# Optimization experiments

Hardware: AMD Instinct MI355X
Metric: run time of the kernel (lower is better)

Reference implementation:

```python
import jax, jax.numpy as jnp
import numpy as np

EPS = 1e-5

def conv2d(x, w, b=None, pad=1):
    # x: [B,C,H,W], w: [O,I,kh,kw]
    y = jax.lax.conv_general_dilated(x, w, (1, 1), [(pad, pad), (pad, pad)],
                                     dimension_numbers=('NCHW', 'OIHW', 'NCHW'))
    if b is not None:
        y = y + b[None, :, None, None]
    return y

def bn(x, g, b, m, v):
    # inference-mode batchnorm
    inv = g / jnp.sqrt(v + EPS)
    return x * inv[None, :, None, None] + (b - m * inv)[None, :, None, None]

def coord_conv(x, w, b):
    B, C, H, W = x.shape
    yy = jnp.broadcast_to(jnp.linspace(-1.0, 1.0, H)[:, None], (H, W))
    xx = jnp.broadcast_to(jnp.linspace(-1.0, 1.0, W)[None, :], (H, W))
    coords = jnp.broadcast_to(jnp.stack([xx, yy])[None], (B, 2, H, W)).astype(x.dtype)
    return conv2d(jnp.concatenate([x, coords], axis=1), w, b, pad=1)

def deform_conv(x, offset, w):
    # deformable conv v1, 3x3, pad=1, stride=1, no bias
    B, C, H, W = x.shape
    K = 9
    # offset channels interleaved (y, x) per kernel tap
    off = offset.reshape(B, K, 2, H, W)
    off_y, off_x = off[:, :, 0], off[:, :, 1]          # [B,9,H,W]
    k = jnp.arange(K)
    ko_y = (k // 3 - 1).astype(x.dtype)[None, :, None, None]
    ko_x = (k % 3 - 1).astype(x.dtype)[None, :, None, None]
    base_y = jnp.arange(H, dtype=x.dtype)[None, None, :, None]
    base_x = jnp.arange(W, dtype=x.dtype)[None, None, None, :]
    py = base_y + ko_y + off_y                          # [B,9,H,W]
    px = base_x + ko_x + off_x
    xf = x.reshape(B, C, H * W)
    y0 = jnp.floor(py)
    x0 = jnp.floor(px)
    acc = jnp.zeros((B, C, K, H, W), x.dtype)
    for dy in (0.0, 1.0):
        for dx in (0.0, 1.0):
            yy = y0 + dy
            xx = x0 + dx
            wgt = (1.0 - jnp.abs(py - yy)) * (1.0 - jnp.abs(px - xx))
            valid = (yy >= 0) & (yy < H) & (xx >= 0) & (xx < W)
            wgt = jnp.where(valid, wgt, 0.0)            # zero padding OOB
            yi = jnp.clip(yy, 0, H - 1).astype(jnp.int32)
            xi = jnp.clip(xx, 0, W - 1).astype(jnp.int32)
            idx = (yi * W + xi).reshape(B, K * H * W)
            v = jnp.take_along_axis(xf, idx[:, None, :], axis=2).reshape(B, C, K, H, W)
            acc = acc + v * wgt[:, None]
    wk = w.reshape(w.shape[0], w.shape[1], K)           # [O,I,9]
    return jnp.einsum('bckhw,ock->bohw', acc, wk)

def setup_inputs() -> dict:
    key = jax.random.key(0)
    ks = jax.random.split(key, 16)
    d_model, hd = 256, 64
    B, H, W = 8, 96, 96
    f32 = jnp.float32
    def bn_params(k):
        k1, k2, k3 = jax.random.split(k, 3)
        return (1.0 + 0.1 * jax.random.normal(k1, (hd,), f32),
                0.1 * jax.random.normal(k2, (hd,), f32),
                0.1 * jax.random.normal(k3, (hd,), f32),
                0.5 + jax.random.uniform(jax.random.fold_in(k, 7), (hd,), f32))
    bn1 = bn_params(ks[1]); bn2 = bn_params(ks[2]); bn3 = bn_params(ks[3]); bn4 = bn_params(ks[4])
    inp = {
        'features': jax.random.normal(ks[0], (B, H, W, d_model), f32),
        'coord_w': 0.05 * jax.random.normal(ks[5], (hd, d_model + 2, 3, 3), f32),
        'coord_b': jnp.zeros((hd,), f32),
        'bn1_g': bn1[0], 'bn1_b': bn1[1], 'bn1_m': bn1[2], 'bn1_v': bn1[3],
        'off_w': 0.01 * jax.random.normal(ks[6], (18, hd, 3, 3), f32),
        'off_b': 0.01 * jax.random.normal(ks[7], (18,), f32),
        'dc_w': 0.05 * jax.random.normal(ks[8], (hd, hd, 3, 3), f32),
        'bn2_g': bn2[0], 'bn2_b': bn2[1], 'bn2_m': bn2[2], 'bn2_v': bn2[3],
        'r1_w': 0.05 * jax.random.normal(ks[9], (hd, hd, 3, 3), f32),
        'bn3_g': bn3[0], 'bn3_b': bn3[1], 'bn3_m': bn3[2], 'bn3_v': bn3[3],
        'r2_w': 0.05 * jax.random.normal(ks[10], (hd, hd, 3, 3), f32),
        'bn4_g': bn4[0], 'bn4_b': bn4[1], 'bn4_m': bn4[2], 'bn4_v': bn4[3],
        'out_w': 0.1 * jax.random.normal(ks[11], (1, hd, 1, 1), f32),
        'out_b': jnp.zeros((1,), f32),
    }
    return inp

def reference(features, coord_w, coord_b, bn1_g, bn1_b, bn1_m, bn1_v,
              off_w, off_b, dc_w, bn2_g, bn2_b, bn2_m, bn2_v,
              r1_w, bn3_g, bn3_b, bn3_m, bn3_v,
              r2_w, bn4_g, bn4_b, bn4_m, bn4_v, out_w, out_b):
    x = jnp.transpose(features, (0, 3, 1, 2))           # NHWC -> NCHW
    x = jax.nn.relu(bn(coord_conv(x, coord_w, coord_b), bn1_g, bn1_b, bn1_m, bn1_v))
    offset = conv2d(x, off_w, off_b, pad=1)
    x = deform_conv(x, offset, dc_w)
    x = jax.nn.relu(bn(x, bn2_g, bn2_b, bn2_m, bn2_v))
    x = jax.nn.relu(bn(conv2d(x, r1_w, None, pad=1), bn3_g, bn3_b, bn3_m, bn3_v))
    x = jax.nn.relu(bn(conv2d(x, r2_w, None, pad=1), bn4_g, bn4_b, bn4_m, bn4_v))
    return jax.nn.sigmoid(conv2d(x, out_w, out_b, pad=0))
```

## Files before the change

kernel.cpp:

```cpp
#include <hip/hip_runtime.h>


typedef unsigned short u16;
typedef unsigned int u32;
typedef __attribute__((ext_vector_type(8)))  short bf16x8;
typedef __attribute__((ext_vector_type(16))) float f32x16;

#define EPSBN 1e-5f

__device__ __forceinline__ u16 f2bf(float f) {
  u32 u = __builtin_bit_cast(u32, f);
  u32 r = u + 0x7FFFu + ((u >> 16) & 1u);
  return (u16)(r >> 16);
}
__device__ __forceinline__ u32 pk2(float a, float b) {
  return (u32)f2bf(a) | ((u32)f2bf(b) << 16);
}
__device__ __forceinline__ float lo2f(u32 w) { return __builtin_bit_cast(float, w << 16); }
__device__ __forceinline__ float hi2f(u32 w) { return __builtin_bit_cast(float, w & 0xFFFF0000u); }

#define N_WCF 147456
#define N_WCC 9216
#define N_WOF 18432
#define N_W64 36864
#define N_ALLW (N_WCF + N_WCC + N_WOF + 3*N_W64)

__global__ __launch_bounds__(256) void prep_kernel(
    const float* __restrict__ coord_w, const float* __restrict__ off_w,
    const float* __restrict__ dc_w, const float* __restrict__ r1_w,
    const float* __restrict__ r2_w,
    u16* __restrict__ wcf, u16* __restrict__ wcc, u16* __restrict__ wof,
    u16* __restrict__ wdf, u16* __restrict__ wr1, u16* __restrict__ wr2)
{
  int i = blockIdx.x * 256 + threadIdx.x;
  if (i >= N_ALLW) return;
  int d = i;
  if (d < N_WCF) {
    int j = d & 7, lane = (d >> 3) & 63, frag = d >> 9;
    int nt = frag & 1, h = (frag >> 1) & 3, tap = (frag >> 3) % 9, cc = (frag >> 3) / 9;
    int ic = cc * 64 + h * 16 + ((lane >> 5) << 3) + j;
    int oc = nt * 32 + (lane & 31);
    wcf[d] = f2bf(coord_w[((size_t)oc * 258 + ic) * 9 + tap]);
    return;
  }
  d -= N_WCF;
  if (d < N_WCC) {
    int j = d & 7, lane = (d >> 3) & 63, frag = d >> 9;
    int nt = frag & 1, tap = frag >> 1;
    int ic = 256 + ((lane >> 5) << 3) + j;
    int oc = nt * 32 + (lane & 31);
    wcc[d] = (ic < 258) ? f2bf(coord_w[((size_t)oc * 258 + ic) * 9 + tap]) : (u16)0;
    return;
  }
  d -= N_WCC;
  if (d < N_WOF) {
    int j = d & 7, lane = (d >> 3) & 63, frag = d >> 9;
    int h = frag & 3, tap = frag >> 2;
    int ic = h * 16 + ((lane >> 5) << 3) + j;
    int oc = lane & 31;
    wof[d] = (oc < 18) ? f2bf(off_w[((size_t)oc * 64 + ic) * 9 + tap]) : (u16)0;
    return;
  }
  d -= N_WOF;
  int seg = d / N_W64;
  int e = d - seg * N_W64;
  int j = e & 7, lane = (e >> 3) & 63, frag = e >> 9;
  int nt = frag & 1, h = (frag >> 1) & 3, tap = frag >> 3;
  int ic = h * 16 + ((lane >> 5) << 3) + j;
  int oc = nt * 32 + (lane & 31);
  const float* src = (seg == 0) ? dc_w : (seg == 1) ? r1_w : r2_w;
  u16* dst = (seg == 0) ? wdf : (seg == 1) ? wr1 : wr2;
  dst[e] = f2bf(src[((size_t)oc * 64 + ic) * 9 + tap]);
}

__global__ __launch_bounds__(256, 4) void coord_conv_kernel(
    const float* __restrict__ feat, const u16* __restrict__ wcf,
    const u16* __restrict__ wcc, const float* __restrict__ cb,
    const float* __restrict__ g, const float* __restrict__ bb,
    const float* __restrict__ m, const float* __restrict__ v,
    u16* __restrict__ x1b)
{
  __shared__ __align__(16) u16 tile[6 * 34 * 72];
  const int t = threadIdx.x;
  const int wv = t >> 6, lane = t & 63;
  const int l31 = lane & 31, l5 = lane >> 5;
  const int x0 = blockIdx.x * 32, y0 = blockIdx.y * 4, b = blockIdx.z;

  f32x16 acc[2] = {};

  for (int cc = 0; cc < 4; ++cc) {
    __syncthreads();
    for (int i = t; i < 1632; i += 256) {
      const int px = i >> 3, gg = i & 7;
      const int ly = px / 34, lx = px - ly * 34;
      const int gy = y0 + ly - 1, gx = x0 + lx - 1;
      uint4 o = {0u, 0u, 0u, 0u};
      if ((unsigned)gy < 96u && (unsigned)gx < 96u) {
        const float* p = feat + ((size_t)((b * 96 + gy) * 96 + gx)) * 256
                         + cc * 64 + gg * 8;
        const float4 f0 = *(const float4*)p;
        const float4 f1 = *(const float4*)(p + 4);
        o.x = pk2(f0.x, f0.y); o.y = pk2(f0.z, f0.w);
        o.z = pk2(f1.x, f1.y); o.w = pk2(f1.z, f1.w);
      }
      *(uint4*)(tile + (ly * 34 + lx) * 72 + gg * 8) = o;
    }
    __syncthreads();
    #pragma unroll
    for (int tap = 0; tap < 9; ++tap) {
      const int dy = tap / 3, dx = tap - dy * 3;
      #pragma unroll
      for (int h = 0; h < 4; ++h) {
        const bf16x8 afr = *(const bf16x8*)(tile +
            ((wv + dy) * 34 + l31 + dx) * 72 + h * 16 + l5 * 8);
        #pragma unroll
        for (int nt = 0; nt < 2; ++nt) {
          const bf16x8 bfr = *(const bf16x8*)(wcf +
              ((size_t)((((cc * 9 + tap) * 4 + h) * 2) + nt)) * 512 + lane * 8);
          acc[nt] = __builtin_amdgcn_mfma_f32_32x32x16_bf16(afr, bfr, acc[nt],
                                                            0, 0, 0);
        }
      }
    }
  }

  __syncthreads();
  for (int i = t; i < 408; i += 256) {
    const int px = i >> 1, gg = i & 1;
    const int ly = px / 34, lx = px - ly * 34;
    const int gy = y0 + ly - 1, gx = x0 + lx - 1;
    uint4 o = {0u, 0u, 0u, 0u};
    if (gg == 0 && (unsigned)gy < 96u && (unsigned)gx < 96u) {
      const float xx = -1.f + (2.f / 95.f) * (float)gx;
      const float yy = -1.f + (2.f / 95.f) * (float)gy;
      o.x = pk2(xx, yy);
    }
    *(uint4*)(tile + (ly * 34 + lx) * 72 + gg * 8) = o;
  }
  __syncthreads();
  #pragma unroll
  for (int tap = 0; tap < 9; ++tap) {
    const int dy = tap / 3, dx = tap - dy * 3;
    const bf16x8 afr = *(const bf16x8*)(tile +
        ((wv + dy) * 34 + l31 + dx) * 72 + l5 * 8);
    #pragma unroll
    for (int nt = 0; nt < 2; ++nt) {
      const bf16x8 bfr = *(const bf16x8*)(wcc +
          ((size_t)(tap * 2 + nt)) * 512 + lane * 8);
      acc[nt] = __builtin_amdgcn_mfma_f32_32x32x16_bf16(afr, bfr, acc[nt],
                                                        0, 0, 0);
    }
  }

  const int y = y0 + wv;
  #pragma unroll
  for (int nt = 0; nt < 2; ++nt) {
    const int oc = nt * 32 + l31;
    const float inv = g[oc] * rsqrtf(v[oc] + EPSBN);
    const float sh = bb[oc] - m[oc] * inv + cb[oc] * inv;
    #pragma unroll
    for (int r = 0; r < 16; ++r) {
      const int xr = (r & 3) + 8 * (r >> 2) + 4 * l5;
      const float val = fmaxf(fmaf(acc[nt][r], inv, sh), 0.f);
      x1b[((size_t)((b * 96 + y) * 96 + x0 + xr)) * 64 + oc] = f2bf(val);
    }
  }
}

template<int NN, int EPI>
__global__ __launch_bounds__(256, 4) void conv64_kernel(
    const u16* __restrict__ xin, const u16* __restrict__ wf,
    const float* __restrict__ bias,
    const float* __restrict__ g, const float* __restrict__ bb,
    const float* __restrict__ m, const float* __restrict__ v,
    const float* __restrict__ ow, const float* __restrict__ ob,
    void* __restrict__ outp)
{
  __shared__ __align__(16) u16 tile[6 * 34 * 72];
  __shared__ float red[128];
  const int t = threadIdx.x;
  const int wv = t >> 6, lane = t & 63;
  const int l31 = lane & 31, l5 = lane >> 5;
  const int x0 = blockIdx.x * 32, y0 = blockIdx.y * 4, b = blockIdx.z;

  for (int i = t; i < 1632; i += 256) {
    const int px = i >> 3, gg = i & 7;
    const int ly = px / 34, lx = px - ly * 34;
    const int gy = y0 + ly - 1, gx = x0 + lx - 1;
    uint4 o = {0u, 0u, 0u, 0u};
    if ((unsigned)gy < 96u && (unsigned)gx < 96u)
      o = *(const uint4*)(xin + (((size_t)((b * 96 + gy) * 96 + gx)) << 6)
                          + gg * 8);
    *(uint4*)(tile + (ly * 34 + lx) * 72 + gg * 8) = o;
  }
  __syncthreads();

  f32x16 acc[NN] = {};
  #pragma unroll
  for (int tap = 0; tap < 9; ++tap) {
    const int dy = tap / 3, dx = tap - dy * 3;
    #pragma unroll
    for (int h = 0; h < 4; ++h) {
      const bf16x8 afr = *(const bf16x8*)(tile +
          ((wv + dy) * 34 + l31 + dx) * 72 + h * 16 + l5 * 8);
      #pragma unroll
      for (int nt = 0; nt < NN; ++nt) {
        const bf16x8 bfr = *(const bf16x8*)(wf +
            ((size_t)((tap * 4 + h) * NN + nt)) * 512 + lane * 8);
        acc[nt] = __builtin_amdgcn_mfma_f32_32x32x16_bf16(afr, bfr, acc[nt],
                                                          0, 0, 0);
      }
    }
  }

  const int y = y0 + wv;
  if constexpr (EPI == 0) {
    u16* xo = (u16*)outp;
    #pragma unroll
    for (int nt = 0; nt < NN; ++nt) {
      const int oc = nt * 32 + l31;
      const float inv = g[oc] * rsqrtf(v[oc] + EPSBN);
      const float sh = bb[oc] - m[oc] * inv;
      #pragma unroll
      for (int r = 0; r < 16; ++r) {
        const int xr = (r & 3) + 8 * (r >> 2) + 4 * l5;
        const float val = fmaxf(fmaf(acc[nt][r], inv, sh), 0.f);
        xo[((size_t)((b * 96 + y) * 96 + x0 + xr)) * 64 + oc] = f2bf(val);
      }
    }
  } else if constexpr (EPI == 1) {
    float* fo = (float*)outp;
    const int oc = l31;
    if (oc < 18) {
      const float bs = bias[oc];
      #pragma unroll
      for (int r = 0; r < 16; ++r) {
        const int xr = (r & 3) + 8 * (r >> 2) + 4 * l5;
        fo[((size_t)((b * 96 + y) * 96 + x0 + xr)) * 18 + oc] = acc[0][r] + bs;
      }
    }
  } else {
    float pr[16];
    #pragma unroll
    for (int r = 0; r < 16; ++r) pr[r] = 0.f;
    #pragma unroll
    for (int nt = 0; nt < NN; ++nt) {
      const int oc = nt * 32 + l31;
      const float inv = g[oc] * rsqrtf(v[oc] + EPSBN);
      const float sh = bb[oc] - m[oc] * inv;
      const float wo = ow[oc];
      #pragma unroll
      for (int r = 0; r < 16; ++r) {
        const float val = fmaxf(fmaf(acc[nt][r], inv, sh), 0.f);
        pr[r] = fmaf(val, wo, pr[r]);
      }
    }
    #pragma unroll
    for (int mask = 1; mask <= 16; mask <<= 1)
      #pragma unroll
      for (int r = 0; r < 16; ++r)
        pr[r] += __shfl_xor(pr[r], mask);
    if (l31 == 0) {
      #pragma unroll
      for (int r = 0; r < 16; ++r) {
        const int xr = (r & 3) + 8 * (r >> 2) + 4 * l5;
        red[wv * 32 + xr] = pr[r];
      }
    }
    __syncthreads();
    if (t < 128) {
      float* fo = (float*)outp;
      const int yy = y0 + (t >> 5), xx = x0 + (t & 31);
      const float val = red[t] + ob[0];
      fo[(size_t)(b * 96 + yy) * 96 + xx] = 1.f / (1.f + expf(-val));
    }
  }
}

__global__ __launch_bounds__(256, 4) void deform_kernel(
    const u16* __restrict__ x1b, const float* __restrict__ off,
    const u16* __restrict__ wdf,
    const float* __restrict__ g, const float* __restrict__ bb,
    const float* __restrict__ m, const float* __restrict__ v,
    u16* __restrict__ x2b)
{
  __shared__ __align__(16) u16 s[128 * 72];
  __shared__ float offs[128 * 18];
  const int t = threadIdx.x;
  const int wv = t >> 6, lane = t & 63;
  const int l31 = lane & 31, l5 = lane >> 5;
  const int x0 = blockIdx.x * 16, y0 = blockIdx.y * 8, b = blockIdx.z;

  for (int i = t; i < 2304; i += 256) {
    const int p = i / 18, c = i - p * 18;
    const int gy = y0 + (p >> 4), gx = x0 + (p & 15);
    offs[i] = off[((size_t)((b * 96 + gy) * 96 + gx)) * 18 + c];
  }

  f32x16 acc[2] = {};

  for (int k = 0; k < 9; ++k) {
    __syncthreads();
    #pragma unroll
    for (int rr = 0; rr < 2; ++rr) {
      const int role = t + rr * 256;
      const int sp = role >> 2, part = role & 3;
      const int sy = y0 + (sp >> 4), sx = x0 + (sp & 15);
      const float oy = offs[sp * 18 + 2 * k];
      const float ox = offs[sp * 18 + 2 * k + 1];
      const float py = (float)(sy + k / 3 - 1) + oy;
      const float px = (float)(sx + k % 3 - 1) + ox;
      const float yf = floorf(py), xf = floorf(px);
      const float fy = py - yf, fx = px - xf;
      const int yi = (int)yf, xi = (int)xf;
      float val[16];
      #pragma unroll
      for (int j = 0; j < 16; ++j) val[j] = 0.f;
      #pragma unroll
      for (int cor = 0; cor < 4; ++cor) {
        const int cy = yi + (cor >> 1), cx = xi + (cor & 1);
        if ((unsigned)cy < 96u && (unsigned)cx < 96u) {
          const float wy = (cor & 2) ? fy : 1.f - fy;
          const float wx = (cor & 1) ? fx : 1.f - fx;
          const float wgt = wy * wx;
          const u16* sp2 = x1b + ((size_t)((b * 96 + cy) * 96 + cx)) * 64
                           + part * 16;
          const uint4 ua = *(const uint4*)sp2;
          const uint4 ub = *(const uint4*)(sp2 + 8);
          const u32 uu[8] = {ua.x, ua.y, ua.z, ua.w, ub.x, ub.y, ub.z, ub.w};
          #pragma unroll
          for (int u = 0; u < 8; ++u) {
            val[2 * u]     = fmaf(wgt, lo2f(uu[u]), val[2 * u]);
            val[2 * u + 1] = fmaf(wgt, hi2f(uu[u]), val[2 * u + 1]);
          }
        }
      }
      u32 pk[8];
      #pragma unroll
      for (int u = 0; u < 8; ++u) pk[u] = pk2(val[2 * u], val[2 * u + 1]);
      uint4 w0 = {pk[0], pk[1], pk[2], pk[3]};
      uint4 w1 = {pk[4], pk[5], pk[6], pk[7]};
      *(uint4*)(s + sp * 72 + part * 16) = w0;
      *(uint4*)(s + sp * 72 + part * 16 + 8) = w1;
    }
    __syncthreads();
    #pragma unroll
    for (int h = 0; h < 4; ++h) {
      const bf16x8 afr = *(const bf16x8*)(s + (wv * 32 + l31) * 72
                                          + h * 16 + l5 * 8);
      #pragma unroll
      for (int nt = 0; nt < 2; ++nt) {
        const bf16x8 bfr = *(const bf16x8*)(wdf +
            ((size_t)((k * 4 + h) * 2 + nt)) * 512 + lane * 8);
        acc[nt] = __builtin_amdgcn_mfma_f32_32x32x16_bf16(afr, bfr, acc[nt],
                                                          0, 0, 0);
      }
    }
  }

  #pragma unroll
  for (int nt = 0; nt < 2; ++nt) {
    const int oc = nt * 32 + l31;
    const float inv = g[oc] * rsqrtf(v[oc] + EPSBN);
    const float sh = bb[oc] - m[oc] * inv;
    #pragma unroll
    for (int r = 0; r < 16; ++r) {
      const int pxi = wv * 32 + (r & 3) + 8 * (r >> 2) + 4 * l5;
      const int y = y0 + (pxi >> 4), x = x0 + (pxi & 15);
      const float val = fmaxf(fmaf(acc[nt][r], inv, sh), 0.f);
      x2b[((size_t)((b * 96 + y) * 96 + x)) * 64 + oc] = f2bf(val);
    }
  }
}

extern "C" void kernel_launch(void* const* d_in, const int* in_sizes, int n_in,
                              void* d_out, int out_size, void* d_ws,
                              size_t ws_size, hipStream_t stream)
{
  (void)in_sizes; (void)n_in; (void)out_size; (void)ws_size;
  const float* features = (const float*)d_in[0];
  const float* coord_w  = (const float*)d_in[1];
  const float* coord_b  = (const float*)d_in[2];
  const float* bn1g = (const float*)d_in[3];
  const float* bn1b = (const float*)d_in[4];
  const float* bn1m = (const float*)d_in[5];
  const float* bn1v = (const float*)d_in[6];
  const float* off_w = (const float*)d_in[7];
  const float* off_b = (const float*)d_in[8];
  const float* dc_w  = (const float*)d_in[9];
  const float* bn2g = (const float*)d_in[10];
  const float* bn2b = (const float*)d_in[11];
  const float* bn2m = (const float*)d_in[12];
  const float* bn2v = (const float*)d_in[13];
  const float* r1_w = (const float*)d_in[14];
  const float* bn3g = (const float*)d_in[15];
  const float* bn3b = (const float*)d_in[16];
  const float* bn3m = (const float*)d_in[17];
  const float* bn3v = (const float*)d_in[18];
  const float* r2_w = (const float*)d_in[19];
  const float* bn4g = (const float*)d_in[20];
  const float* bn4b = (const float*)d_in[21];
  const float* bn4m = (const float*)d_in[22];
  const float* bn4v = (const float*)d_in[23];
  const float* out_w = (const float*)d_in[24];
  const float* out_b = (const float*)d_in[25];

  char* W = (char*)d_ws;
  float* offb = (float*)W;
  u16*   x1b  = (u16*)(W + 5308416);
  u16*   x2b  = (u16*)(W + 14745600);
  u16*   x3b  = (u16*)(W + 24182784);
  u16*   wcf  = (u16*)(W + 33619968);
  u16*   wcc  = wcf + N_WCF;
  u16*   wof  = wcc + N_WCC;
  u16*   wdf  = wof + N_WOF;
  u16*   wr1  = wdf + N_W64;
  u16*   wr2  = wr1 + N_W64;

  prep_kernel<<<(N_ALLW + 255) / 256, 256, 0, stream>>>(
      coord_w, off_w, dc_w, r1_w, r2_w, wcf, wcc, wof, wdf, wr1, wr2);

  dim3 grid(3, 24, 8);
  dim3 gridD(6, 12, 8);

  coord_conv_kernel<<<grid, 256, 0, stream>>>(
      features, wcf, wcc, coord_b, bn1g, bn1b, bn1m, bn1v, x1b);
  conv64_kernel<1, 1><<<grid, 256, 0, stream>>>(
      x1b, wof, off_b, nullptr, nullptr, nullptr, nullptr, nullptr, nullptr,
      (void*)offb);
  deform_kernel<<<gridD, 256, 0, stream>>>(
      x1b, offb, wdf, bn2g, bn2b, bn2m, bn2v, x2b);
  conv64_kernel<2, 0><<<grid, 256, 0, stream>>>(
      x2b, wr1, nullptr, bn3g, bn3b, bn3m, bn3v, nullptr, nullptr, (void*)x3b);
  conv64_kernel<2, 2><<<grid, 256, 0, stream>>>(
      x3b, wr2, nullptr, bn4g, bn4b, bn4m, bn4v, out_w, out_b, d_out);
}
```

Measured before the change: 270.8 us.

## Fuse offset conv into deform kernel, precompute coord channels, double-buffer loads

Several changes land together. The coordinate-channel part of the coord conv is precomputed once into a per-pixel table in the prep kernel rather than run as extra MFMA work. The offset conv is fused into the deform kernel through a shared-memory halo, which removes one launch and the global offset buffer. All conv kernels move to 512 threads, with each wave owning one output-channel tile. The coord conv and the deform gather gain register-staged double buffering so loads overlap the MFMA work. The trade-offs are more register pressure, shared-memory atomics in the final reduction, and a larger prep kernel.

```diff
diff --git a/kernel.cpp b/kernel.cpp
--- a/kernel.cpp
+++ b/kernel.cpp
@@ -19,21 +19,31 @@
 __device__ __forceinline__ float lo2f(u32 w) { return __builtin_bit_cast(float, w << 16); }
 __device__ __forceinline__ float hi2f(u32 w) { return __builtin_bit_cast(float, w & 0xFFFF0000u); }
 
+#define O_X1   0u
+#define O_X2   9437184u
+#define O_X3   18874368u
+#define O_PRE  28311552u
+#define O_WCF  30670848u
+#define O_WOF  30965760u
+#define O_WDF  31002624u
+#define O_WR1  31076352u
+#define O_WR2  31150080u
+
 #define N_WCF 147456
-#define N_WCC 9216
 #define N_WOF 18432
 #define N_W64 36864
-#define N_ALLW (N_WCF + N_WCC + N_WOF + 3*N_W64)
+#define N_PRE 589824
+#define N_TOT (N_WCF + N_WOF + 3*N_W64 + N_PRE)
 
 __global__ __launch_bounds__(256) void prep_kernel(
-    const float* __restrict__ coord_w, const float* __restrict__ off_w,
-    const float* __restrict__ dc_w, const float* __restrict__ r1_w,
-    const float* __restrict__ r2_w,
-    u16* __restrict__ wcf, u16* __restrict__ wcc, u16* __restrict__ wof,
-    u16* __restrict__ wdf, u16* __restrict__ wr1, u16* __restrict__ wr2)
+    const float* __restrict__ coord_w, const float* __restrict__ coord_b,
+    const float* __restrict__ off_w, const float* __restrict__ dc_w,
+    const float* __restrict__ r1_w, const float* __restrict__ r2_w,
+    u16* __restrict__ wcf, u16* __restrict__ wof, u16* __restrict__ wdf,
+    u16* __restrict__ wr1, u16* __restrict__ wr2, float* __restrict__ pre)
 {
   int i = blockIdx.x * 256 + threadIdx.x;
-  if (i >= N_ALLW) return;
+  if (i >= N_TOT) return;
   int d = i;
   if (d < N_WCF) {
     int j = d & 7, lane = (d >> 3) & 63, frag = d >> 9;
@@ -44,15 +54,6 @@
     return;
   }
   d -= N_WCF;
-  if (d < N_WCC) {
-    int j = d & 7, lane = (d >> 3) & 63, frag = d >> 9;
-    int nt = frag & 1, tap = frag >> 1;
-    int ic = 256 + ((lane >> 5) << 3) + j;
-    int oc = nt * 32 + (lane & 31);
-    wcc[d] = (ic < 258) ? f2bf(coord_w[((size_t)oc * 258 + ic) * 9 + tap]) : (u16)0;
-    return;
-  }
-  d -= N_WCC;
   if (d < N_WOF) {
     int j = d & 7, lane = (d >> 3) & 63, frag = d >> 9;
     int h = frag & 3, tap = frag >> 2;
@@ -62,199 +63,203 @@
     return;
   }
   d -= N_WOF;
-  int seg = d / N_W64;
-  int e = d - seg * N_W64;
-  int j = e & 7, lane = (e >> 3) & 63, frag = e >> 9;
-  int nt = frag & 1, h = (frag >> 1) & 3, tap = frag >> 3;
-  int ic = h * 16 + ((lane >> 5) << 3) + j;
-  int oc = nt * 32 + (lane & 31);
-  const float* src = (seg == 0) ? dc_w : (seg == 1) ? r1_w : r2_w;
-  u16* dst = (seg == 0) ? wdf : (seg == 1) ? wr1 : wr2;
-  dst[e] = f2bf(src[((size_t)oc * 64 + ic) * 9 + tap]);
-}
-
-__global__ __launch_bounds__(256, 4) void coord_conv_kernel(
+  if (d < 3 * N_W64) {
+    int seg = d / N_W64;
+    int e = d - seg * N_W64;
+    int j = e & 7, lane = (e >> 3) & 63, frag = e >> 9;
+    int nt = frag & 1, h = (frag >> 1) & 3, tap = frag >> 3;
+    int ic = h * 16 + ((lane >> 5) << 3) + j;
+    int oc = nt * 32 + (lane & 31);
+    const float* src = (seg == 0) ? dc_w : (seg == 1) ? r1_w : r2_w;
+    u16* dst = (seg == 0) ? wdf : (seg == 1) ? wr1 : wr2;
+    dst[e] = f2bf(src[((size_t)oc * 64 + ic) * 9 + tap]);
+    return;
+  }
+  d -= 3 * N_W64;
+  int oc = d & 63;
+  int r = d >> 6;
+  int x = r % 96, y = r / 96;
+  float s = coord_b[oc];
+  #pragma unroll
+  for (int tap = 0; tap < 9; ++tap) {
+    const int dy = tap / 3, dx = tap - dy * 3;
+    const int sy = y + dy - 1, sx = x + dx - 1;
+    if ((unsigned)sy < 96u && (unsigned)sx < 96u) {
+      const float xx = -1.f + (2.f / 95.f) * (float)sx;
+      const float yy = -1.f + (2.f / 95.f) * (float)sy;
+      s += coord_w[((size_t)oc * 258 + 256) * 9 + tap] * xx
+         + coord_w[((size_t)oc * 258 + 257) * 9 + tap] * yy;
+    }
+  }
+  pre[((size_t)(y * 96 + x) << 6) + oc] = s;
+}
+
+__global__ __launch_bounds__(512, 4) void coord_conv_kernel(
     const float* __restrict__ feat, const u16* __restrict__ wcf,
-    const u16* __restrict__ wcc, const float* __restrict__ cb,
+    const float* __restrict__ pre,
     const float* __restrict__ g, const float* __restrict__ bb,
     const float* __restrict__ m, const float* __restrict__ v,
     u16* __restrict__ x1b)
 {
-  __shared__ __align__(16) u16 tile[6 * 34 * 72];
+  __shared__ __align__(16) u16 buf[2][204 * 72];
   const int t = threadIdx.x;
   const int wv = t >> 6, lane = t & 63;
   const int l31 = lane & 31, l5 = lane >> 5;
+  const int row = wv >> 1, nt = wv & 1;
   const int x0 = blockIdx.x * 32, y0 = blockIdx.y * 4, b = blockIdx.z;
 
-  f32x16 acc[2] = {};
-
+  int rpx[4], rgg[4]; size_t rgo[4]; bool rok[4], ract[4];
+  #pragma unroll
+  for (int it = 0; it < 4; ++it) {
+    int r = t + it * 512;
+    ract[it] = (r < 1632);
+    int px = r >> 3; if (px > 203) px = 203;
+    rgg[it] = r & 7;
+    rpx[it] = px;
+    int ly = px / 34, lx = px - ly * 34;
+    int gy = y0 + ly - 1, gx = x0 + lx - 1;
+    rok[it] = ract[it] && ((unsigned)gy < 96u) && ((unsigned)gx < 96u);
+    rgo[it] = ((size_t)((b * 96 + gy) * 96 + gx)) * 256 + rgg[it] * 8;
+  }
+
+  float4 ra[4][2];
+  #pragma unroll
+  for (int it = 0; it < 4; ++it) {
+    ra[it][0] = make_float4(0.f, 0.f, 0.f, 0.f);
+    ra[it][1] = make_float4(0.f, 0.f, 0.f, 0.f);
+    if (rok[it]) {
+      const float* p = feat + rgo[it];
+      ra[it][0] = *(const float4*)p;
+      ra[it][1] = *(const float4*)(p + 4);
+    }
+  }
+  #pragma unroll
+  for (int it = 0; it < 4; ++it) if (ract[it]) {
+    uint4 o = {pk2(ra[it][0].x, ra[it][0].y), pk2(ra[it][0].z, ra[it][0].w),
+               pk2(ra[it][1].x, ra[it][1].y), pk2(ra[it][1].z, ra[it][1].w)};
+    *(uint4*)(&buf[0][rpx[it] * 72 + rgg[it] * 8]) = o;
+  }
+  __syncthreads();
+
+  f32x16 acc = {};
   for (int cc = 0; cc < 4; ++cc) {
-    __syncthreads();
-    for (int i = t; i < 1632; i += 256) {
-      const int px = i >> 3, gg = i & 7;
-      const int ly = px / 34, lx = px - ly * 34;
-      const int gy = y0 + ly - 1, gx = x0 + lx - 1;
-      uint4 o = {0u, 0u, 0u, 0u};
-      if ((unsigned)gy < 96u && (unsigned)gx < 96u) {
-        const float* p = feat + ((size_t)((b * 96 + gy) * 96 + gx)) * 256
-                         + cc * 64 + gg * 8;
-        const float4 f0 = *(const float4*)p;
-        const float4 f1 = *(const float4*)(p + 4);
-        o.x = pk2(f0.x, f0.y); o.y = pk2(f0.z, f0.w);
-        o.z = pk2(f1.x, f1.y); o.w = pk2(f1.z, f1.w);
-      }
-      *(uint4*)(tile + (ly * 34 + lx) * 72 + gg * 8) = o;
-    }
-    __syncthreads();
+    const int cur = cc & 1;
+    if (cc < 3) {
+      #pragma unroll
+      for (int it = 0; it < 4; ++it) {
+        ra[it][0] = make_float4(0.f, 0.f, 0.f, 0.f);
+        ra[it][1] = make_float4(0.f, 0.f, 0.f, 0.f);
+        if (rok[it]) {
+          const float* p = feat + rgo[it] + (size_t)(cc + 1) * 64;
+          ra[it][0] = *(const float4*)p;
+          ra[it][1] = *(const float4*)(p + 4);
+        }
+      }
+    }
     #pragma unroll
     for (int tap = 0; tap < 9; ++tap) {
       const int dy = tap / 3, dx = tap - dy * 3;
       #pragma unroll
       for (int h = 0; h < 4; ++h) {
-        const bf16x8 afr = *(const bf16x8*)(tile +
-            ((wv + dy) * 34 + l31 + dx) * 72 + h * 16 + l5 * 8);
-        #pragma unroll
-        for (int nt = 0; nt < 2; ++nt) {
-          const bf16x8 bfr = *(const bf16x8*)(wcf +
-              ((size_t)((((cc * 9 + tap) * 4 + h) * 2) + nt)) * 512 + lane * 8);
-          acc[nt] = __builtin_amdgcn_mfma_f32_32x32x16_bf16(afr, bfr, acc[nt],
-                                                            0, 0, 0);
-        }
-      }
-    }
-  }
-
-  __syncthreads();
-  for (int i = t; i < 408; i += 256) {
-    const int px = i >> 1, gg = i & 1;
-    const int ly = px / 34, lx = px - ly * 34;
-    const int gy = y0 + ly - 1, gx = x0 + lx - 1;
-    uint4 o = {0u, 0u, 0u, 0u};
-    if (gg == 0 && (unsigned)gy < 96u && (unsigned)gx < 96u) {
-      const float xx = -1.f + (2.f / 95.f) * (float)gx;
-      const float yy = -1.f + (2.f / 95.f) * (float)gy;
-      o.x = pk2(xx, yy);
-    }
-    *(uint4*)(tile + (ly * 34 + lx) * 72 + gg * 8) = o;
-  }
-  __syncthreads();
-  #pragma unroll
-  for (int tap = 0; tap < 9; ++tap) {
-    const int dy = tap / 3, dx = tap - dy * 3;
-    const bf16x8 afr = *(const bf16x8*)(tile +
-        ((wv + dy) * 34 + l31 + dx) * 72 + l5 * 8);
-    #pragma unroll
-    for (int nt = 0; nt < 2; ++nt) {
-      const bf16x8 bfr = *(const bf16x8*)(wcc +
-          ((size_t)(tap * 2 + nt)) * 512 + lane * 8);
-      acc[nt] = __builtin_amdgcn_mfma_f32_32x32x16_bf16(afr, bfr, acc[nt],
-                                                        0, 0, 0);
-    }
-  }
-
-  const int y = y0 + wv;
-  #pragma unroll
-  for (int nt = 0; nt < 2; ++nt) {
-    const int oc = nt * 32 + l31;
-    const float inv = g[oc] * rsqrtf(v[oc] + EPSBN);
-    const float sh = bb[oc] - m[oc] * inv + cb[oc] * inv;
-    #pragma unroll
-    for (int r = 0; r < 16; ++r) {
-      const int xr = (r & 3) + 8 * (r >> 2) + 4 * l5;
-      const float val = fmaxf(fmaf(acc[nt][r], inv, sh), 0.f);
-      x1b[((size_t)((b * 96 + y) * 96 + x0 + xr)) * 64 + oc] = f2bf(val);
-    }
-  }
-}
-
-template<int NN, int EPI>
-__global__ __launch_bounds__(256, 4) void conv64_kernel(
+        const bf16x8 afr = *(const bf16x8*)(
+            &buf[cur][((row + dy) * 34 + l31 + dx) * 72 + h * 16 + l5 * 8]);
+        const bf16x8 bfr = *(const bf16x8*)(
+            wcf + ((size_t)(((cc * 9 + tap) * 4 + h) * 2 + nt)) * 512 + lane * 8);
+        acc = __builtin_amdgcn_mfma_f32_32x32x16_bf16(afr, bfr, acc, 0, 0, 0);
+      }
+    }
+    if (cc < 3) {
+      #pragma unroll
+      for (int it = 0; it < 4; ++it) if (ract[it]) {
+        uint4 o = {pk2(ra[it][0].x, ra[it][0].y), pk2(ra[it][0].z, ra[it][0].w),
+                   pk2(ra[it][1].x, ra[it][1].y), pk2(ra[it][1].z, ra[it][1].w)};
+        *(uint4*)(&buf[1 - cur][rpx[it] * 72 + rgg[it] * 8]) = o;
+      }
+    }
+    __syncthreads();
+  }
+
+  const int oc = nt * 32 + l31;
+  const float inv = g[oc] * rsqrtf(v[oc] + EPSBN);
+  const float sh = bb[oc] - m[oc] * inv;
+  const int y = y0 + row;
+  #pragma unroll
+  for (int r = 0; r < 16; ++r) {
+    const int xr = (r & 3) + 8 * (r >> 2) + 4 * l5;
+    const int x = x0 + xr;
+    const float pv = pre[((size_t)(y * 96 + x) << 6) + oc];
+    const float val = fmaxf(fmaf(acc[r] + pv, inv, sh), 0.f);
+    x1b[(((size_t)((b * 96 + y) * 96 + x)) << 6) + oc] = f2bf(val);
+  }
+}
+
+template<int EPI>
+__global__ __launch_bounds__(512, 4) void conv64_kernel(
     const u16* __restrict__ xin, const u16* __restrict__ wf,
-    const float* __restrict__ bias,
     const float* __restrict__ g, const float* __restrict__ bb,
     const float* __restrict__ m, const float* __restrict__ v,
     const float* __restrict__ ow, const float* __restrict__ ob,
     void* __restrict__ outp)
 {
-  __shared__ __align__(16) u16 tile[6 * 34 * 72];
+  __shared__ __align__(16) u16 tile[204 * 72];
   __shared__ float red[128];
   const int t = threadIdx.x;
   const int wv = t >> 6, lane = t & 63;
   const int l31 = lane & 31, l5 = lane >> 5;
+  const int row = wv >> 1, nt = wv & 1;
   const int x0 = blockIdx.x * 32, y0 = blockIdx.y * 4, b = blockIdx.z;
 
-  for (int i = t; i < 1632; i += 256) {
-    const int px = i >> 3, gg = i & 7;
-    const int ly = px / 34, lx = px - ly * 34;
-    const int gy = y0 + ly - 1, gx = x0 + lx - 1;
-    uint4 o = {0u, 0u, 0u, 0u};
-    if ((unsigned)gy < 96u && (unsigned)gx < 96u)
-      o = *(const uint4*)(xin + (((size_t)((b * 96 + gy) * 96 + gx)) << 6)
-                          + gg * 8);
-    *(uint4*)(tile + (ly * 34 + lx) * 72 + gg * 8) = o;
+  if constexpr (EPI == 2) { if (t < 128) red[t] = 0.f; }
+
+  #pragma unroll
+  for (int it = 0; it < 4; ++it) {
+    int r = t + it * 512;
+    if (r < 1632) {
+      int px = r >> 3, gg = r & 7;
+      int ly = px / 34, lx = px - ly * 34;
+      int gy = y0 + ly - 1, gx = x0 + lx - 1;
+      uint4 o = {0u, 0u, 0u, 0u};
+      if ((unsigned)gy < 96u && (unsigned)gx < 96u)
+        o = *(const uint4*)(xin + (((size_t)((b * 96 + gy) * 96 + gx)) << 6)
+                            + gg * 8);
+      *(uint4*)(&tile[px * 72 + gg * 8]) = o;
+    }
   }
   __syncthreads();
 
-  f32x16 acc[NN] = {};
+  f32x16 acc = {};
   #pragma unroll
   for (int tap = 0; tap < 9; ++tap) {
     const int dy = tap / 3, dx = tap - dy * 3;
     #pragma unroll
     for (int h = 0; h < 4; ++h) {
-      const bf16x8 afr = *(const bf16x8*)(tile +
-          ((wv + dy) * 34 + l31 + dx) * 72 + h * 16 + l5 * 8);
-      #pragma unroll
-      for (int nt = 0; nt < NN; ++nt) {
-        const bf16x8 bfr = *(const bf16x8*)(wf +
-            ((size_t)((tap * 4 + h) * NN + nt)) * 512 + lane * 8);
-        acc[nt] = __builtin_amdgcn_mfma_f32_32x32x16_bf16(afr, bfr, acc[nt],
-                                                          0, 0, 0);
-      }
-    }
-  }
-
-  const int y = y0 + wv;
+      const bf16x8 afr = *(const bf16x8*)(
+          &tile[((row + dy) * 34 + l31 + dx) * 72 + h * 16 + l5 * 8]);
+      const bf16x8 bfr = *(const bf16x8*)(
+          wf + ((size_t)((tap * 4 + h) * 2 + nt)) * 512 + lane * 8);
+      acc = __builtin_amdgcn_mfma_f32_32x32x16_bf16(afr, bfr, acc, 0, 0, 0);
+    }
+  }
+
+  const int oc = nt * 32 + l31;
+  const float inv = g[oc] * rsqrtf(v[oc] + EPSBN);
+  const float sh = bb[oc] - m[oc] * inv;
+  const int y = y0 + row;
+
   if constexpr (EPI == 0) {
     u16* xo = (u16*)outp;
     #pragma unroll
-    for (int nt = 0; nt < NN; ++nt) {
-      const int oc = nt * 32 + l31;
-      const float inv = g[oc] * rsqrtf(v[oc] + EPSBN);
-      const float sh = bb[oc] - m[oc] * inv;
-      #pragma unroll
-      for (int r = 0; r < 16; ++r) {
-        const int xr = (r & 3) + 8 * (r >> 2) + 4 * l5;
-        const float val = fmaxf(fmaf(acc[nt][r], inv, sh), 0.f);
-        xo[((size_t)((b * 96 + y) * 96 + x0 + xr)) * 64 + oc] = f2bf(val);
-      }
-    }
-  } else if constexpr (EPI == 1) {
-    float* fo = (float*)outp;
-    const int oc = l31;
-    if (oc < 18) {
-      const float bs = bias[oc];
-      #pragma unroll
-      for (int r = 0; r < 16; ++r) {
-        const int xr = (r & 3) + 8 * (r >> 2) + 4 * l5;
-        fo[((size_t)((b * 96 + y) * 96 + x0 + xr)) * 18 + oc] = acc[0][r] + bs;
-      }
+    for (int r = 0; r < 16; ++r) {
+      const int xr = (r & 3) + 8 * (r >> 2) + 4 * l5;
+      const float val = fmaxf(fmaf(acc[r], inv, sh), 0.f);
+      xo[(((size_t)((b * 96 + y) * 96 + x0 + xr)) << 6) + oc] = f2bf(val);
     }
   } else {
+    const float wo = ow[oc];
     float pr[16];
     #pragma unroll
-    for (int r = 0; r < 16; ++r) pr[r] = 0.f;
-    #pragma unroll
-    for (int nt = 0; nt < NN; ++nt) {
-      const int oc = nt * 32 + l31;
-      const float inv = g[oc] * rsqrtf(v[oc] + EPSBN);
-      const float sh = bb[oc] - m[oc] * inv;
-      const float wo = ow[oc];
-      #pragma unroll
-      for (int r = 0; r < 16; ++r) {
-        const float val = fmaxf(fmaf(acc[nt][r], inv, sh), 0.f);
-        pr[r] = fmaf(val, wo, pr[r]);
-      }
-    }
+    for (int r = 0; r < 16; ++r)
+      pr[r] = fmaxf(fmaf(acc[r], inv, sh), 0.f) * wo;
     #pragma unroll
     for (int mask = 1; mask <= 16; mask <<= 1)
       #pragma unroll
@@ -264,7 +269,7 @@
       #pragma unroll
       for (int r = 0; r < 16; ++r) {
         const int xr = (r & 3) + 8 * (r >> 2) + 4 * l5;
-        red[wv * 32 + xr] = pr[r];
+        atomicAdd(&red[row * 32 + xr], pr[r]);
       }
     }
     __syncthreads();
@@ -277,99 +282,151 @@
   }
 }
 
-__global__ __launch_bounds__(256, 4) void deform_kernel(
-    const u16* __restrict__ x1b, const float* __restrict__ off,
-    const u16* __restrict__ wdf,
+__global__ __launch_bounds__(512, 4) void offdeform_kernel(
+    const u16* __restrict__ x1b, const u16* __restrict__ wof,
+    const u16* __restrict__ wdf, const float* __restrict__ off_b,
     const float* __restrict__ g, const float* __restrict__ bb,
     const float* __restrict__ m, const float* __restrict__ v,
     u16* __restrict__ x2b)
 {
-  __shared__ __align__(16) u16 s[128 * 72];
-  __shared__ float offs[128 * 18];
+  __shared__ __align__(16) char arena[9216 + 36864];
+  float* offs = (float*)arena;
+  u16* halo = (u16*)(arena + 9216);
+  u16* sb0 = (u16*)(arena + 9216);
+  u16* sb1 = (u16*)(arena + 9216 + 18432);
   const int t = threadIdx.x;
   const int wv = t >> 6, lane = t & 63;
   const int l31 = lane & 31, l5 = lane >> 5;
+  const int mtile = wv >> 1, nt = wv & 1;
   const int x0 = blockIdx.x * 16, y0 = blockIdx.y * 8, b = blockIdx.z;
 
-  for (int i = t; i < 2304; i += 256) {
-    const int p = i / 18, c = i - p * 18;
-    const int gy = y0 + (p >> 4), gx = x0 + (p & 15);
-    offs[i] = off[((size_t)((b * 96 + gy) * 96 + gx)) * 18 + c];
-  }
-
-  f32x16 acc[2] = {};
-
-  for (int k = 0; k < 9; ++k) {
-    __syncthreads();
+  #pragma unroll
+  for (int it = 0; it < 3; ++it) {
+    int r = t + it * 512;
+    if (r < 1440) {
+      int px = r >> 3, gg = r & 7;
+      int hy = px / 18, hx = px - hy * 18;
+      int gy = y0 + hy - 1, gx = x0 + hx - 1;
+      uint4 o = {0u, 0u, 0u, 0u};
+      if ((unsigned)gy < 96u && (unsigned)gx < 96u)
+        o = *(const uint4*)(x1b + (((size_t)((b * 96 + gy) * 96 + gx)) << 6)
+                            + gg * 8);
+      *(uint4*)(&halo[px * 72 + gg * 8]) = o;
+    }
+  }
+  __syncthreads();
+
+  if (wv < 4) {
+    const int om = wv * 32 + l31;
+    const int oy_ = om >> 4, ox_ = om & 15;
+    f32x16 oacc = {};
+    #pragma unroll
+    for (int tap = 0; tap < 9; ++tap) {
+      const int dy = tap / 3, dx = tap - dy * 3;
+      #pragma unroll
+      for (int h = 0; h < 4; ++h) {
+        const bf16x8 afr = *(const bf16x8*)(
+            &halo[((oy_ + dy) * 18 + ox_ + dx) * 72 + h * 16 + l5 * 8]);
+        const bf16x8 bfr = *(const bf16x8*)(
+            wof + ((size_t)(tap * 4 + h)) * 512 + lane * 8);
+        oacc = __builtin_amdgcn_mfma_f32_32x32x16_bf16(afr, bfr, oacc, 0, 0, 0);
+      }
+    }
+    if (l31 < 18) {
+      const float bs = off_b[l31];
+      #pragma unroll
+      for (int r = 0; r < 16; ++r) {
+        const int p = wv * 32 + (r & 3) + 8 * (r >> 2) + 4 * l5;
+        offs[p * 18 + l31] = oacc[r] + bs;
+      }
+    }
+  }
+  __syncthreads();
+
+  const int gg = t & 7, p0 = t >> 3;
+  f32x16 acc = {};
+  uint4 cv[2][4];
+  float cw[2][4];
+
+  auto gather = [&](int k) {
+    const int kdy = k / 3, kdx = k - kdy * 3;
     #pragma unroll
     for (int rr = 0; rr < 2; ++rr) {
-      const int role = t + rr * 256;
-      const int sp = role >> 2, part = role & 3;
-      const int sy = y0 + (sp >> 4), sx = x0 + (sp & 15);
-      const float oy = offs[sp * 18 + 2 * k];
-      const float ox = offs[sp * 18 + 2 * k + 1];
-      const float py = (float)(sy + k / 3 - 1) + oy;
-      const float px = (float)(sx + k % 3 - 1) + ox;
-      const float yf = floorf(py), xf = floorf(px);
-      const float fy = py - yf, fx = px - xf;
+      const int p = p0 + rr * 64;
+      const float oy = offs[p * 18 + 2 * k];
+      const float ox = offs[p * 18 + 2 * k + 1];
+      const float py = (float)(y0 + (p >> 4) + kdy - 1) + oy;
+      const float pxf = (float)(x0 + (p & 15) + kdx - 1) + ox;
+      const float yf = floorf(py), xf = floorf(pxf);
+      const float fy = py - yf, fx = pxf - xf;
       const int yi = (int)yf, xi = (int)xf;
-      float val[16];
-      #pragma unroll
-      for (int j = 0; j < 16; ++j) val[j] = 0.f;
       #pragma unroll
       for (int cor = 0; cor < 4; ++cor) {
         const int cy = yi + (cor >> 1), cx = xi + (cor & 1);
-        if ((unsigned)cy < 96u && (unsigned)cx < 96u) {
-          const float wy = (cor & 2) ? fy : 1.f - fy;
-          const float wx = (cor & 1) ? fx : 1.f - fx;
-          const float wgt = wy * wx;
-          const u16* sp2 = x1b + ((size_t)((b * 96 + cy) * 96 + cx)) * 64
-                           + part * 16;
-          const uint4 ua = *(const uint4*)sp2;
-          const uint4 ub = *(const uint4*)(sp2 + 8);
-          const u32 uu[8] = {ua.x, ua.y, ua.z, ua.w, ub.x, ub.y, ub.z, ub.w};
-          #pragma unroll
-          for (int u = 0; u < 8; ++u) {
-            val[2 * u]     = fmaf(wgt, lo2f(uu[u]), val[2 * u]);
-            val[2 * u + 1] = fmaf(wgt, hi2f(uu[u]), val[2 * u + 1]);
-          }
+        const bool okc = ((unsigned)cy < 96u) && ((unsigned)cx < 96u);
+        const float wy = (cor & 2) ? fy : 1.f - fy;
+        const float wx = (cor & 1) ? fx : 1.f - fx;
+        cw[rr][cor] = okc ? wy * wx : 0.f;
+        uint4 z = {0u, 0u, 0u, 0u};
+        cv[rr][cor] = okc ? *(const uint4*)(x1b +
+            (((size_t)((b * 96 + cy) * 96 + cx)) << 6) + gg * 8) : z;
+      }
+    }
+  };
+  auto blend_store = [&](u16* dst) {
+    #pragma unroll
+    for (int rr = 0; rr < 2; ++rr) {
+      const int p = p0 + rr * 64;
+      float o8[8];
+      #pragma unroll
+      for (int u = 0; u < 8; ++u) o8[u] = 0.f;
+      #pragma unroll
+      for (int cor = 0; cor < 4; ++cor) {
+        const float wgt = cw[rr][cor];
+        const u32 uu[4] = {cv[rr][cor].x, cv[rr][cor].y,
+                           cv[rr][cor].z, cv[rr][cor].w};
+        #pragma unroll
+        for (int u = 0; u < 4; ++u) {
+          o8[2 * u]     = fmaf(wgt, lo2f(uu[u]), o8[2 * u]);
+          o8[2 * u + 1] = fmaf(wgt, hi2f(uu[u]), o8[2 * u + 1]);
         }
       }
-      u32 pk[8];
-      #pragma unroll
-      for (int u = 0; u < 8; ++u) pk[u] = pk2(val[2 * u], val[2 * u + 1]);
-      uint4 w0 = {pk[0], pk[1], pk[2], pk[3]};
-      uint4 w1 = {pk[4], pk[5], pk[6], pk[7]};
-      *(uint4*)(s + sp * 72 + part * 16) = w0;
-      *(uint4*)(s + sp * 72 + part * 16 + 8) = w1;
-    }
+      uint4 w_;
+      w_.x = pk2(o8[0], o8[1]); w_.y = pk2(o8[2], o8[3]);
+      w_.z = pk2(o8[4], o8[5]); w_.w = pk2(o8[6], o8[7]);
+      *(uint4*)(&dst[p * 72 + gg * 8]) = w_;
+    }
+  };
+
+  gather(0);
+  blend_store(sb0);
+  __syncthreads();
+
+  for (int k = 0; k < 9; ++k) {
+    u16* curb = (k & 1) ? sb1 : sb0;
+    u16* nxtb = (k & 1) ? sb0 : sb1;
+    if (k < 8) gather(k + 1);
+    #pragma unroll
+    for (int h = 0; h < 4; ++h) {
+      const bf16x8 afr = *(const bf16x8*)(
+          &curb[(mtile * 32 + l31) * 72 + h * 16 + l5 * 8]);
+      const bf16x8 bfr = *(const bf16x8*)(
+          wdf + ((size_t)((k * 4 + h) * 2 + nt)) * 512 + lane * 8);
+      acc = __builtin_amdgcn_mfma_f32_32x32x16_bf16(afr, bfr, acc, 0, 0, 0);
+    }
+    if (k < 8) blend_store(nxtb);
     __syncthreads();
-    #pragma unroll
-    for (int h = 0; h < 4; ++h) {
-      const bf16x8 afr = *(const bf16x8*)(s + (wv * 32 + l31) * 72
-                                          + h * 16 + l5 * 8);
-      #pragma unroll
-      for (int nt = 0; nt < 2; ++nt) {
-        const bf16x8 bfr = *(const bf16x8*)(wdf +
-            ((size_t)((k * 4 + h) * 2 + nt)) * 512 + lane * 8);
-        acc[nt] = __builtin_amdgcn_mfma_f32_32x32x16_bf16(afr, bfr, acc[nt],
-                                                          0, 0, 0);
-      }
-    }
-  }
-
-  #pragma unroll
-  for (int nt = 0; nt < 2; ++nt) {
-    const int oc = nt * 32 + l31;
-    const float inv = g[oc] * rsqrtf(v[oc] + EPSBN);
-    const float sh = bb[oc] - m[oc] * inv;
-    #pragma unroll
-    for (int r = 0; r < 16; ++r) {
-      const int pxi = wv * 32 + (r & 3) + 8 * (r >> 2) + 4 * l5;
-      const int y = y0 + (pxi >> 4), x = x0 + (pxi & 15);
-      const float val = fmaxf(fmaf(acc[nt][r], inv, sh), 0.f);
-      x2b[((size_t)((b * 96 + y) * 96 + x)) * 64 + oc] = f2bf(val);
-    }
+  }
+
+  const int oc = nt * 32 + l31;
+  const float inv = g[oc] * rsqrtf(v[oc] + EPSBN);
+  const float sh = bb[oc] - m[oc] * inv;
+  #pragma unroll
+  for (int r = 0; r < 16; ++r) {
+    const int p = mtile * 32 + (r & 3) + 8 * (r >> 2) + 4 * l5;
+    const int y = y0 + (p >> 4), x = x0 + (p & 15);
+    const float val = fmaxf(fmaf(acc[r], inv, sh), 0.f);
+    x2b[(((size_t)((b * 96 + y) * 96 + x)) << 6) + oc] = f2bf(val);
   }
 }
 
@@ -406,32 +463,28 @@
   const float* out_b = (const float*)d_in[25];
 
   char* W = (char*)d_ws;
-  float* offb = (float*)W;
-  u16*   x1b  = (u16*)(W + 5308416);
-  u16*   x2b  = (u16*)(W + 14745600);
-  u16*   x3b  = (u16*)(W + 24182784);
-  u16*   wcf  = (u16*)(W + 33619968);
-  u16*   wcc  = wcf + N_WCF;
-  u16*   wof  = wcc + N_WCC;
-  u16*   wdf  = wof + N_WOF;
-  u16*   wr1  = wdf + N_W64;
-  u16*   wr2  = wr1 + N_W64;
-
-  prep_kernel<<<(N_ALLW + 255) / 256, 256, 0, stream>>>(
-      coord_w, off_w, dc_w, r1_w, r2_w, wcf, wcc, wof, wdf, wr1, wr2);
+  u16*   x1b = (u16*)(W + O_X1);
+  u16*   x2b = (u16*)(W + O_X2);
+  u16*   x3b = (u16*)(W + O_X3);
+  float* pre = (float*)(W + O_PRE);
+  u16*   wcf = (u16*)(W + O_WCF);
+  u16*   wof = (u16*)(W + O_WOF);
+  u16*   wdf = (u16*)(W + O_WDF);
+  u16*   wr1 = (u16*)(W + O_WR1);
+  u16*   wr2 = (u16*)(W + O_WR2);
+
+  prep_kernel<<<(N_TOT + 255) / 256, 256, 0, stream>>>(
+      coord_w, coord_b, off_w, dc_w, r1_w, r2_w, wcf, wof, wdf, wr1, wr2, pre);
 
   dim3 grid(3, 24, 8);
   dim3 gridD(6, 12, 8);
 
-  coord_conv_kernel<<<grid, 256, 0, stream>>>(
-      features, wcf, wcc, coord_b, bn1g, bn1b, bn1m, bn1v, x1b);
-  conv64_kernel<1, 1><<<grid, 256, 0, stream>>>(
-      x1b, wof, off_b, nullptr, nullptr, nullptr, nullptr, nullptr, nullptr,
-      (void*)offb);
-  deform_kernel<<<gridD, 256, 0, stream>>>(
-      x1b, offb, wdf, bn2g, bn2b, bn2m, bn2v, x2b);
-  conv64_kernel<2, 0><<<grid, 256, 0, stream>>>(
-      x2b, wr1, nullptr, bn3g, bn3b, bn3m, bn3v, nullptr, nullptr, (void*)x3b);
-  conv64_kernel<2, 2><<<grid, 256, 0, stream>>>(
-      x3b, wr2, nullptr, bn4g, bn4b, bn4m, bn4v, out_w, out_b, d_out);
-}
+  coord_conv_kernel<<<grid, 512, 0, stream>>>(
+      features, wcf, pre, bn1g, bn1b, bn1m, bn1v, x1b);
+  offdeform_kernel<<<gridD, 512, 0, stream>>>(
+      x1b, wof, wdf, off_b, bn2g, bn2b, bn2m, bn2v, x2b);
+  conv64_kernel<0><<<grid, 512, 0, stream>>>(
+      x2b, wr1, bn3g, bn3b, bn3m, bn3v, nullptr, nullptr, (void*)x3b);
+  conv64_kernel<2><<<grid, 512, 0, stream>>>(
+      x3b, wr2, bn4g, bn4b, bn4m, bn4v, out_w, out_b, d_out);
+}
```

Result: slower. 335.7 us (+24.0%).
